# Kernel tuning notes

Measured on AMD Instinct MI355X. Metric: run time of the kernel, lower is better.

The kernel has to match this reference:

```python
import jax, jax.numpy as jnp
import numpy as np

N_ITEMS = 7000
N_USERS = 30000
N_NODES = N_ITEMS + N_USERS  # 37000
D = 128        # embed_dim == user_embed_dim
E = 400000     # num edges
R = 10         # n_relation (num ratings)
NB = 8         # num_bases
B = 512        # batch of conversations
L = 100        # max context items per sample


def setup_inputs() -> dict:
    key = jax.random.key(0)
    ks = jax.random.split(key, 16)
    # edges: item (source) -> user (target), disjoint id ranges as in load_data
    src = jax.random.randint(ks[0], (E,), 0, N_ITEMS)
    dst = jax.random.randint(ks[1], (E,), N_ITEMS, N_NODES)
    edge_index = jnp.stack([src, dst]).astype(jnp.int64)
    edge_type = jax.random.randint(ks[2], (E,), 0, R).astype(jnp.int64)

    def make_ctx(k1, k2):
        c = jax.random.randint(k1, (B, L), 0, N_ITEMS)
        drop = jax.random.uniform(k2, (B, L)) < 0.3  # -1 padding as in batch lists
        return jnp.where(drop, -1, c).astype(jnp.int64)

    ctx_init = make_ctx(ks[3], ks[4])
    ctx_resp = make_ctx(ks[5], ks[6])

    s = 0.02
    basis = jax.random.normal(ks[7], (NB, N_NODES, D), jnp.float32) * s
    comp = jax.random.normal(ks[8], (R, NB), jnp.float32) * s
    root = jax.random.normal(ks[9], (N_NODES, D), jnp.float32) * s
    bias = jnp.zeros((D,), jnp.float32)
    attn_a = jax.random.normal(ks[10], (D, D), jnp.float32) * s
    attn_b = jax.random.normal(ks[11], (D,), jnp.float32) * s
    fc1_w = jax.random.normal(ks[12], (D, D), jnp.float32) * s
    fc1_b = jnp.zeros((D,), jnp.float32)
    fc2_w = jax.random.normal(ks[13], (D, D), jnp.float32) * s
    fc2_b = jnp.zeros((D,), jnp.float32)
    efc1_w = jax.random.normal(ks[14], (2 * D, D), jnp.float32) * s
    efc1_b = jnp.zeros((D,), jnp.float32)
    efc2_w = jax.random.normal(ks[15], (D, D), jnp.float32) * s
    efc2_b = jnp.zeros((D,), jnp.float32)
    return dict(edge_index=edge_index, edge_type=edge_type, ctx_init=ctx_init,
                ctx_resp=ctx_resp, basis=basis, comp=comp, root=root, bias=bias,
                attn_a=attn_a, attn_b=attn_b, fc1_w=fc1_w, fc1_b=fc1_b,
                fc2_w=fc2_w, fc2_b=fc2_b, efc1_w=efc1_w, efc1_b=efc1_b,
                efc2_w=efc2_w, efc2_b=efc2_b)


def _rgcn(basis, comp, root, bias, edge_index, edge_type):
    # RGCNConv with x=None: per-edge message W_{r_e}[src_e], mean-aggregated
    # per (target, relation), summed over relations, plus root lookup + bias.
    src, dst = edge_index[0], edge_index[1]
    nb, n, d = basis.shape
    r = comp.shape[0]
    cpe = comp[edge_type]  # [E, NB]
    msg = jnp.zeros((src.shape[0], d), basis.dtype)
    for b in range(nb):  # small fixed basis count; avoids [E,NB,D] gather
        msg = msg + cpe[:, b:b + 1] * basis[b][src]
    seg = dst * r + edge_type  # per-(node, relation) segment for mean aggr
    sums = jax.ops.segment_sum(msg, seg, num_segments=n * r).reshape(n, r, d)
    cnt = jax.ops.segment_sum(jnp.ones_like(edge_type, basis.dtype), seg,
                              num_segments=n * r).reshape(n, r, 1)
    return root + bias + (sums / jnp.maximum(cnt, 1.0)).sum(axis=1)  # [N, D]


def _item_user_means(node_emb, edge_index):
    # mean over users connected to each item (edge_idx[1][edge_idx[0]==item])
    src, dst = edge_index[0], edge_index[1]
    isum = jax.ops.segment_sum(node_emb[dst], src, num_segments=N_ITEMS)
    icnt = jax.ops.segment_sum(jnp.ones_like(src, node_emb.dtype), src,
                               num_segments=N_ITEMS)
    item_mean = isum / jnp.maximum(icnt, 1.0)[:, None]  # [N_ITEMS, D]
    return item_mean, icnt > 0


def _attn_pool(ctx, item_mean, item_has_users, attn_a, attn_b):
    # SelfAttentionBatch over each sample's item reps (padding/-1 & degree-0
    # items masked out; all-empty samples -> zeros, as in original).
    valid = ctx >= 0
    idx = jnp.clip(ctx, 0, N_ITEMS - 1)
    h = item_mean[idx]                       # [B, L, D]
    valid = valid & item_has_users[idx]
    e = jnp.einsum('bld,d->bl', jnp.tanh(jnp.einsum('bld,de->ble', h, attn_a)),
                   attn_b)
    attn = jax.nn.softmax(jnp.where(valid, e, -1e9), axis=-1)
    attn = jnp.where(valid, attn, 0.0)
    return jnp.einsum('bl,bld->bd', attn, h)  # [B, D]


def _project(x, w1, b1, w2, b2):
    # fc1 -> relu -> fc2 -> relu (as in _project_user_interaction_*)
    return jax.nn.relu(jax.nn.relu(x @ w1 + b1) @ w2 + b2)


def reference(edge_index, edge_type, ctx_init, ctx_resp, basis, comp, root,
              bias, attn_a, attn_b, fc1_w, fc1_b, fc2_w, fc2_b, efc1_w,
              efc1_b, efc2_w, efc2_b):
    node_emb = _rgcn(basis, comp, root, bias, edge_index, edge_type)
    item_mean, item_has = _item_user_means(node_emb, edge_index)
    p_init = _project(_attn_pool(ctx_init, item_mean, item_has, attn_a, attn_b),
                      fc1_w, fc1_b, fc2_w, fc2_b)
    p_resp = _project(_attn_pool(ctx_resp, item_mean, item_has, attn_a, attn_b),
                      fc1_w, fc1_b, fc2_w, fc2_b)
    both = jnp.concatenate([p_init, p_resp], axis=1)  # [B, 2D]
    profile = _project(both, efc1_w, efc1_b, efc2_w, efc2_b)  # [B, D]
    return profile, p_init, p_resp
```

## Files before the change

### kernel.cpp

```cpp
#include <hip/hip_runtime.h>
#include <math.h>

typedef unsigned int uint;

#define N_ITEMS 7000
#define N_NODES 37000
#define N_USERS 30000
#define DIM     128
#define HD      64
#define NREL    10
#define NBASES  8
#define BATCH   512
#define CTXL    100
#define E_MAX   400000

#define OFF_CNT    0
#define OFF_ICNT   (OFF_CNT + N_USERS * NREL)
#define OFF_UCNT   (OFF_ICNT + N_ITEMS)
#define ZERO_ELEMS (OFF_UCNT + N_USERS)
#define OFF_ICUR   ZERO_ELEMS
#define OFF_UCUR   (OFF_ICUR + N_ITEMS)
#define OFF_ICSR   (OFF_UCUR + N_USERS)
#define OFF_UCSR   (OFF_ICSR + E_MAX)
#define OFF_WC     (OFF_UCSR + E_MAX)
#define OFF_ACC    (OFF_WC + NREL * N_ITEMS * HD)
#define OFF_MEAN   (OFF_ACC + N_USERS * HD)
#define OFF_SCORE  (OFF_MEAN + N_ITEMS * HD)

__device__ __forceinline__ float2 bf2f(uint p) {
  float2 r;
  r.x = __uint_as_float(p << 16);
  r.y = __uint_as_float(p & 0xffff0000u);
  return r;
}
__device__ __forceinline__ uint f2bf(float x, float y) {
  uint a = __float_as_uint(x), b = __float_as_uint(y);
  a += 0x7fffu + ((a >> 16) & 1u);
  b += 0x7fffu + ((b >> 16) & 1u);
  return (a >> 16) | (b & 0xffff0000u);
}

__device__ __forceinline__ float wave_sum(float v) {
#pragma unroll
  for (int o = 1; o < 64; o <<= 1) v += __shfl_xor(v, o, 64);
  return v;
}
__device__ __forceinline__ float wave_max(float v) {
#pragma unroll
  for (int o = 1; o < 64; o <<= 1) v = fmaxf(v, __shfl_xor(v, o, 64));
  return v;
}

__global__ __launch_bounds__(HD) void k_combine(const float* __restrict__ basis,
                                                const float* __restrict__ comp,
                                                uint* __restrict__ Wc) {
  int i = blockIdx.x, t = threadIdx.x;
  float2 bb[NBASES];
#pragma unroll
  for (int b = 0; b < NBASES; ++b)
    bb[b] = ((const float2*)(basis + ((size_t)b * N_NODES + i) * DIM))[t];
#pragma unroll
  for (int r = 0; r < NREL; ++r) {
    float sx = 0.f, sy = 0.f;
#pragma unroll
    for (int b = 0; b < NBASES; ++b) {
      float c = comp[r * NBASES + b];
      sx = fmaf(c, bb[b].x, sx);
      sy = fmaf(c, bb[b].y, sy);
    }
    Wc[((size_t)r * N_ITEMS + i) * HD + t] = f2bf(sx, sy);
  }
}

__global__ __launch_bounds__(256) void k_count(const int* __restrict__ ei,
                                               const int* __restrict__ et, int E,
                                               int* __restrict__ cnt,
                                               int* __restrict__ icnt,
                                               int* __restrict__ ucnt) {
  int e = blockIdx.x * 256 + threadIdx.x;
  if (e >= E) return;
  int s = ei[e];
  int u0 = ei[E + e] - N_ITEMS;
  int t = et[e];
  atomicAdd(&cnt[u0 * NREL + t], 1);
  atomicAdd(&icnt[s], 1);
  atomicAdd(&ucnt[u0], 1);
}

__global__ __launch_bounds__(1024) void k_scan(const int* __restrict__ icnt,
                                               const int* __restrict__ ucnt,
                                               int* __restrict__ icur,
                                               int* __restrict__ ucur) {
  __shared__ int ss[1024];
  const int* in;
  int n;
  int* cur;
  if (blockIdx.x == 0) { in = icnt; n = N_ITEMS; cur = icur; }
  else                 { in = ucnt; n = N_USERS; cur = ucur; }
  int t = threadIdx.x;
  int chunk = (n + 1023) / 1024;
  int lo = t * chunk, hi = lo + chunk;
  if (lo > n) lo = n;
  if (hi > n) hi = n;
  int s = 0;
  for (int i = lo; i < hi; ++i) s += in[i];
  ss[t] = s;
  __syncthreads();
  for (int o = 1; o < 1024; o <<= 1) {
    int v = (t >= o) ? ss[t - o] : 0;
    __syncthreads();
    ss[t] += v;
    __syncthreads();
  }
  int base = (t > 0) ? ss[t - 1] : 0;
  for (int i = lo; i < hi; ++i) { cur[i] = base; base += in[i]; }
}

__global__ __launch_bounds__(256) void k_fill(const int* __restrict__ ei,
                                              const int* __restrict__ et, int E,
                                              int* __restrict__ icur,
                                              int* __restrict__ ucur,
                                              int* __restrict__ icsr,
                                              int* __restrict__ ucsr) {
  int e = blockIdx.x * 256 + threadIdx.x;
  if (e >= E) return;
  int s = ei[e];
  int u0 = ei[E + e] - N_ITEMS;
  int t = et[e];
  icsr[atomicAdd(&icur[s], 1)] = u0;
  ucsr[atomicAdd(&ucur[u0], 1)] = s | (t << 16);
}

__global__ __launch_bounds__(HD) void k_useragg(const int* __restrict__ ucnt,
                                                const int* __restrict__ ucur,
                                                const int* __restrict__ ucsr,
                                                const int* __restrict__ cnt,
                                                const uint* __restrict__ Wc,
                                                const float* __restrict__ root,
                                                uint* __restrict__ acc) {
  __shared__ float wrow[NREL];
  __shared__ int sedge[HD];
  int u = blockIdx.x, t = threadIdx.x;
  if (t < NREL) {
    int c = cnt[u * NREL + t];
    wrow[t] = (c > 0) ? 1.0f / (float)c : 0.0f;
  }
  int deg = ucnt[u];
  int base = ucur[u] - deg;
  float2 a0 = {0.f, 0.f}, a1 = {0.f, 0.f}, a2 = {0.f, 0.f}, a3 = {0.f, 0.f};
  for (int j0 = 0; j0 < deg; j0 += HD) {
    int m = deg - j0;
    if (m > HD) m = HD;
    __syncthreads();
    if (t < m) sedge[t] = ucsr[base + j0 + t];
    __syncthreads();
    int j = 0;
    for (; j + 4 <= m; j += 4) {
      int p0 = sedge[j], p1 = sedge[j + 1], p2 = sedge[j + 2], p3 = sedge[j + 3];
      uint q0 = Wc[(size_t)((p0 >> 16) * N_ITEMS + (p0 & 0xffff)) * HD + t];
      uint q1 = Wc[(size_t)((p1 >> 16) * N_ITEMS + (p1 & 0xffff)) * HD + t];
      uint q2 = Wc[(size_t)((p2 >> 16) * N_ITEMS + (p2 & 0xffff)) * HD + t];
      uint q3 = Wc[(size_t)((p3 >> 16) * N_ITEMS + (p3 & 0xffff)) * HD + t];
      float w0 = wrow[p0 >> 16], w1 = wrow[p1 >> 16];
      float w2 = wrow[p2 >> 16], w3 = wrow[p3 >> 16];
      float2 f0 = bf2f(q0), f1 = bf2f(q1), f2 = bf2f(q2), f3 = bf2f(q3);
      a0.x = fmaf(w0, f0.x, a0.x); a0.y = fmaf(w0, f0.y, a0.y);
      a1.x = fmaf(w1, f1.x, a1.x); a1.y = fmaf(w1, f1.y, a1.y);
      a2.x = fmaf(w2, f2.x, a2.x); a2.y = fmaf(w2, f2.y, a2.y);
      a3.x = fmaf(w3, f3.x, a3.x); a3.y = fmaf(w3, f3.y, a3.y);
    }
    for (; j < m; ++j) {
      int p = sedge[j];
      uint q = Wc[(size_t)((p >> 16) * N_ITEMS + (p & 0xffff)) * HD + t];
      float w = wrow[p >> 16];
      float2 f = bf2f(q);
      a0.x = fmaf(w, f.x, a0.x); a0.y = fmaf(w, f.y, a0.y);
    }
  }
  float2 r = ((const float2*)(root + (size_t)(N_ITEMS + u) * DIM))[t];
  r.x += a0.x + a1.x + a2.x + a3.x;
  r.y += a0.y + a1.y + a2.y + a3.y;
  acc[(size_t)u * HD + t] = f2bf(r.x, r.y);
}

__global__ __launch_bounds__(HD) void k_itemagg(const int* __restrict__ icnt,
                                                const int* __restrict__ icur,
                                                const int* __restrict__ icsr,
                                                const uint* __restrict__ acc,
                                                const float* __restrict__ bias,
                                                const float* __restrict__ attn_a,
                                                const float* __restrict__ attn_b,
                                                uint* __restrict__ mean,
                                                float* __restrict__ score) {
  __shared__ int sedge[HD];
  __shared__ float sm[DIM];
  int i = blockIdx.x, t = threadIdx.x;
  int deg = icnt[i];
  int base = icur[i] - deg;
  float2 a0 = {0.f, 0.f}, a1 = {0.f, 0.f}, a2 = {0.f, 0.f}, a3 = {0.f, 0.f};
  for (int j0 = 0; j0 < deg; j0 += HD) {
    int m = deg - j0;
    if (m > HD) m = HD;
    __syncthreads();
    if (t < m) sedge[t] = icsr[base + j0 + t];
    __syncthreads();
    int j = 0;
    for (; j + 4 <= m; j += 4) {
      uint q0 = acc[(size_t)sedge[j] * HD + t];
      uint q1 = acc[(size_t)sedge[j + 1] * HD + t];
      uint q2 = acc[(size_t)sedge[j + 2] * HD + t];
      uint q3 = acc[(size_t)sedge[j + 3] * HD + t];
      float2 f0 = bf2f(q0), f1 = bf2f(q1), f2 = bf2f(q2), f3 = bf2f(q3);
      a0.x += f0.x; a0.y += f0.y;
      a1.x += f1.x; a1.y += f1.y;
      a2.x += f2.x; a2.y += f2.y;
      a3.x += f3.x; a3.y += f3.y;
    }
    for (; j < m; ++j) {
      float2 f = bf2f(acc[(size_t)sedge[j] * HD + t]);
      a0.x += f.x; a0.y += f.y;
    }
  }
  float2 mv = {0.f, 0.f};
  if (deg > 0) {
    float inv = 1.0f / (float)deg;
    float2 bvec = ((const float2*)bias)[t];
    mv.x = (a0.x + a1.x + a2.x + a3.x) * inv + bvec.x;
    mv.y = (a0.y + a1.y + a2.y + a3.y) * inv + bvec.y;
  }
  mean[(size_t)i * HD + t] = f2bf(mv.x, mv.y);
  sm[2 * t] = mv.x;
  sm[2 * t + 1] = mv.y;
  __syncthreads();
  float z0 = 0.f, z1 = 0.f;
#pragma unroll 8
  for (int k = 0; k < DIM; ++k) {
    float2 w = ((const float2*)(attn_a + (size_t)k * DIM))[t];
    float h = sm[k];
    z0 = fmaf(h, w.x, z0);
    z1 = fmaf(h, w.y, z1);
  }
  float2 ab = ((const float2*)attn_b)[t];
  float v = wave_sum(tanhf(z0) * ab.x + tanhf(z1) * ab.y);
  if (t == 0) score[i] = (deg > 0) ? v : -1e9f;
}

__global__ __launch_bounds__(HD) void k_pool(const int* __restrict__ ctx0,
                                             const int* __restrict__ ctx1,
                                             const uint* __restrict__ mean,
                                             const float* __restrict__ score,
                                             const float* __restrict__ fc1_w,
                                             const float* __restrict__ fc1_b,
                                             const float* __restrict__ fc2_w,
                                             const float* __restrict__ fc2_b,
                                             float* __restrict__ out) {
  __shared__ float shw[CTXL];
  __shared__ int shi[CTXL];
  __shared__ float shv[DIM];
  int b = blockIdx.x & (BATCH - 1);
  int c = blockIdx.x >> 9;
  int t = threadIdx.x;
  const int* cx = (c == 0 ? ctx0 : ctx1) + (size_t)b * CTXL;

  int id0 = cx[t];
  float e0 = (id0 >= 0) ? score[id0] : -1e9f;
  int id1 = -1;
  float e1 = -3.0e38f;
  if (t + HD < CTXL) {
    id1 = cx[t + HD];
    e1 = (id1 >= 0) ? score[id1] : -1e9f;
  }
  float m = wave_max(fmaxf(e0, e1));
  float x0 = expf(e0 - m);
  float x1 = (t + HD < CTXL) ? expf(e1 - m) : 0.f;
  float inv = 1.0f / wave_sum(x0 + x1);
  shw[t] = (id0 >= 0) ? x0 * inv : 0.f;
  shi[t] = (id0 >= 0) ? id0 : 0;
  if (t + HD < CTXL) {
    shw[t + HD] = (id1 >= 0) ? x1 * inv : 0.f;
    shi[t + HD] = (id1 >= 0) ? id1 : 0;
  }
  __syncthreads();

  float2 a0 = {0.f, 0.f}, a1 = {0.f, 0.f}, a2 = {0.f, 0.f}, a3 = {0.f, 0.f};
#pragma unroll 5
  for (int l = 0; l < CTXL; l += 4) {
    float w0 = shw[l], w1 = shw[l + 1], w2 = shw[l + 2], w3 = shw[l + 3];
    uint q0 = mean[(size_t)shi[l] * HD + t];
    uint q1 = mean[(size_t)shi[l + 1] * HD + t];
    uint q2 = mean[(size_t)shi[l + 2] * HD + t];
    uint q3 = mean[(size_t)shi[l + 3] * HD + t];
    float2 f0 = bf2f(q0), f1 = bf2f(q1), f2 = bf2f(q2), f3 = bf2f(q3);
    a0.x = fmaf(w0, f0.x, a0.x); a0.y = fmaf(w0, f0.y, a0.y);
    a1.x = fmaf(w1, f1.x, a1.x); a1.y = fmaf(w1, f1.y, a1.y);
    a2.x = fmaf(w2, f2.x, a2.x); a2.y = fmaf(w2, f2.y, a2.y);
    a3.x = fmaf(w3, f3.x, a3.x); a3.y = fmaf(w3, f3.y, a3.y);
  }
  __syncthreads();
  shv[2 * t] = a0.x + a1.x + a2.x + a3.x;
  shv[2 * t + 1] = a0.y + a1.y + a2.y + a3.y;
  __syncthreads();

  float2 z = ((const float2*)fc1_b)[t];
#pragma unroll 8
  for (int k = 0; k < DIM; ++k) {
    float2 w = ((const float2*)(fc1_w + (size_t)k * DIM))[t];
    float h = shv[k];
    z.x = fmaf(h, w.x, z.x);
    z.y = fmaf(h, w.y, z.y);
  }
  z.x = fmaxf(z.x, 0.f);
  z.y = fmaxf(z.y, 0.f);
  __syncthreads();
  shv[2 * t] = z.x;
  shv[2 * t + 1] = z.y;
  __syncthreads();

  float2 z2 = ((const float2*)fc2_b)[t];
#pragma unroll 8
  for (int k = 0; k < DIM; ++k) {
    float2 w = ((const float2*)(fc2_w + (size_t)k * DIM))[t];
    float h = shv[k];
    z2.x = fmaf(h, w.x, z2.x);
    z2.y = fmaf(h, w.y, z2.y);
  }
  z2.x = fmaxf(z2.x, 0.f);
  z2.y = fmaxf(z2.y, 0.f);
  ((float2*)(out + (size_t)(1 + c) * BATCH * DIM + (size_t)b * DIM))[t] = z2;
}

__global__ __launch_bounds__(HD) void k_profile(const float* __restrict__ efc1_w,
                                                const float* __restrict__ efc1_b,
                                                const float* __restrict__ efc2_w,
                                                const float* __restrict__ efc2_b,
                                                float* __restrict__ out) {
  __shared__ float shv[2 * DIM];
  __shared__ float sh2[DIM];
  int b = blockIdx.x, t = threadIdx.x;
  float2 p0 = ((const float2*)(out + (size_t)BATCH * DIM + (size_t)b * DIM))[t];
  float2 p1 = ((const float2*)(out + (size_t)2 * BATCH * DIM + (size_t)b * DIM))[t];
  shv[2 * t] = p0.x;
  shv[2 * t + 1] = p0.y;
  shv[DIM + 2 * t] = p1.x;
  shv[DIM + 2 * t + 1] = p1.y;
  __syncthreads();
  float2 z = ((const float2*)efc1_b)[t];
#pragma unroll 8
  for (int k = 0; k < 2 * DIM; ++k) {
    float2 w = ((const float2*)(efc1_w + (size_t)k * DIM))[t];
    float h = shv[k];
    z.x = fmaf(h, w.x, z.x);
    z.y = fmaf(h, w.y, z.y);
  }
  z.x = fmaxf(z.x, 0.f);
  z.y = fmaxf(z.y, 0.f);
  __syncthreads();
  sh2[2 * t] = z.x;
  sh2[2 * t + 1] = z.y;
  __syncthreads();
  float2 z2 = ((const float2*)efc2_b)[t];
#pragma unroll 8
  for (int k = 0; k < DIM; ++k) {
    float2 w = ((const float2*)(efc2_w + (size_t)k * DIM))[t];
    float h = sh2[k];
    z2.x = fmaf(h, w.x, z2.x);
    z2.y = fmaf(h, w.y, z2.y);
  }
  z2.x = fmaxf(z2.x, 0.f);
  z2.y = fmaxf(z2.y, 0.f);
  ((float2*)(out + (size_t)b * DIM))[t] = z2;
}

extern "C" void kernel_launch(void* const* d_in, const int* in_sizes, int n_in,
                              void* d_out, int out_size, void* d_ws, size_t ws_size,
                              hipStream_t stream) {
  const int*   ei     = (const int*)d_in[0];
  const int*   et     = (const int*)d_in[1];
  const int*   ctx0   = (const int*)d_in[2];
  const int*   ctx1   = (const int*)d_in[3];
  const float* basis  = (const float*)d_in[4];
  const float* comp   = (const float*)d_in[5];
  const float* root   = (const float*)d_in[6];
  const float* bias   = (const float*)d_in[7];
  const float* attn_a = (const float*)d_in[8];
  const float* attn_b = (const float*)d_in[9];
  const float* fc1_w  = (const float*)d_in[10];
  const float* fc1_b  = (const float*)d_in[11];
  const float* fc2_w  = (const float*)d_in[12];
  const float* fc2_b  = (const float*)d_in[13];
  const float* efc1_w = (const float*)d_in[14];
  const float* efc1_b = (const float*)d_in[15];
  const float* efc2_w = (const float*)d_in[16];
  const float* efc2_b = (const float*)d_in[17];
  float* out = (float*)d_out;

  const int E = in_sizes[1];

  float* ws   = (float*)d_ws;
  int*  cnt   = (int*)(ws + OFF_CNT);
  int*  icnt  = (int*)(ws + OFF_ICNT);
  int*  ucnt  = (int*)(ws + OFF_UCNT);
  int*  icur  = (int*)(ws + OFF_ICUR);
  int*  ucur  = (int*)(ws + OFF_UCUR);
  int*  icsr  = (int*)(ws + OFF_ICSR);
  int*  ucsr  = (int*)(ws + OFF_UCSR);
  uint* Wc    = (uint*)(ws + OFF_WC);
  uint* acc   = (uint*)(ws + OFF_ACC);
  uint* mean  = (uint*)(ws + OFF_MEAN);
  float* score = ws + OFF_SCORE;

  hipMemsetAsync(d_ws, 0, (size_t)ZERO_ELEMS * sizeof(float), stream);

  k_combine<<<N_ITEMS, HD, 0, stream>>>(basis, comp, Wc);
  k_count<<<(E + 255) / 256, 256, 0, stream>>>(ei, et, E, cnt, icnt, ucnt);
  k_scan<<<2, 1024, 0, stream>>>(icnt, ucnt, icur, ucur);
  k_fill<<<(E + 255) / 256, 256, 0, stream>>>(ei, et, E, icur, ucur, icsr, ucsr);
  k_useragg<<<N_USERS, HD, 0, stream>>>(ucnt, ucur, ucsr, cnt, Wc, root, acc);
  k_itemagg<<<N_ITEMS, HD, 0, stream>>>(icnt, icur, icsr, acc, bias, attn_a, attn_b,
                                        mean, score);
  k_pool<<<2 * BATCH, HD, 0, stream>>>(ctx0, ctx1, mean, score, fc1_w, fc1_b,
                                       fc2_w, fc2_b, out);
  k_profile<<<BATCH, HD, 0, stream>>>(efc1_w, efc1_b, efc2_w, efc2_b, out);
}
```

Before: 481.3 us.

## Fuse all pipeline stages into one cooperative persistent kernel with grid syncs

Replaces the eight separate launches with a single cooperative kernel of 512 blocks that loops over work per wavefront and separates stages with grid.sync(). The two-block scan becomes a multi-block tiled scan, and the gathers plus small matvecs switch from shared memory to wave shuffles with deeper unrolling of independent accumulators. The aim is to remove launch gaps and per-block sync overhead. In exchange, each stage runs on a fixed grid, which may leave gather-heavy stages with less parallelism or latency hiding than before. The old multi-kernel path is kept as a fallback when cooperative occupancy is insufficient.

```diff
diff --git a/kernel.cpp b/kernel.cpp
--- a/kernel.cpp
+++ b/kernel.cpp
@@ -1,6 +1,8 @@
 #include <hip/hip_runtime.h>
+#include <hip/hip_cooperative_groups.h>
 #include <math.h>
 
+namespace cg = cooperative_groups;
 typedef unsigned int uint;
 
 #define N_ITEMS 7000
@@ -14,13 +16,24 @@
 #define CTXL    100
 #define E_MAX   400000
 
+#define NBLK    512
+#define NTHR    256
+#define NTHREADS_TOT (NBLK * NTHR)
+#define NW      (NTHREADS_TOT / 64)
+
+#define NT_I 28
+#define NT_U 118
+#define NT   (NT_I + NT_U)
+
 #define OFF_CNT    0
 #define OFF_ICNT   (OFF_CNT + N_USERS * NREL)
 #define OFF_UCNT   (OFF_ICNT + N_ITEMS)
 #define ZERO_ELEMS (OFF_UCNT + N_USERS)
 #define OFF_ICUR   ZERO_ELEMS
 #define OFF_UCUR   (OFF_ICUR + N_ITEMS)
-#define OFF_ICSR   (OFF_UCUR + N_USERS)
+#define OFF_TSUM   (OFF_UCUR + N_USERS)
+#define OFF_TOFF   (OFF_TSUM + 256)
+#define OFF_ICSR   (OFF_TOFF + 256)
 #define OFF_UCSR   (OFF_ICSR + E_MAX)
 #define OFF_WC     (OFF_UCSR + E_MAX)
 #define OFF_ACC    (OFF_WC + NREL * N_ITEMS * HD)
@@ -49,6 +62,388 @@
 #pragma unroll
   for (int o = 1; o < 64; o <<= 1) v = fmaxf(v, __shfl_xor(v, o, 64));
   return v;
+}
+__device__ __forceinline__ int wave_sum_i(int v) {
+#pragma unroll
+  for (int o = 1; o < 64; o <<= 1) v += __shfl_xor(v, o, 64);
+  return v;
+}
+
+struct Args {
+  const int* ei;
+  const int* et;
+  const int* ctx0;
+  const int* ctx1;
+  const float* basis;
+  const float* comp;
+  const float* root;
+  const float* bias;
+  const float* attn_a;
+  const float* attn_b;
+  const float* fc1_w;
+  const float* fc1_b;
+  const float* fc2_w;
+  const float* fc2_b;
+  const float* efc1_w;
+  const float* efc1_b;
+  const float* efc2_w;
+  const float* efc2_b;
+  float* out;
+  float* ws;
+  int E;
+};
+
+__global__ __launch_bounds__(NTHR, 2) void k_fused(Args a) {
+  cg::grid_group grid = cg::this_grid();
+  __shared__ int ss[256];
+  __shared__ int s4[4];
+
+  const int tid  = threadIdx.x;
+  const int gtid = blockIdx.x * NTHR + tid;
+  const int wid  = gtid >> 6;
+  const int lane = gtid & 63;
+  const int E = a.E;
+
+  int*  cnt   = (int*)(a.ws + OFF_CNT);
+  int*  icnt  = (int*)(a.ws + OFF_ICNT);
+  int*  ucnt  = (int*)(a.ws + OFF_UCNT);
+  int*  icur  = (int*)(a.ws + OFF_ICUR);
+  int*  ucur  = (int*)(a.ws + OFF_UCUR);
+  int*  tsum  = (int*)(a.ws + OFF_TSUM);
+  int*  toff  = (int*)(a.ws + OFF_TOFF);
+  int*  icsr  = (int*)(a.ws + OFF_ICSR);
+  int*  ucsr  = (int*)(a.ws + OFF_UCSR);
+  uint* Wc    = (uint*)(a.ws + OFF_WC);
+  uint* acc   = (uint*)(a.ws + OFF_ACC);
+  uint* mean  = (uint*)(a.ws + OFF_MEAN);
+  float* score = a.ws + OFF_SCORE;
+
+  const float2* basis2 = (const float2*)a.basis;
+  const float2* root2  = (const float2*)a.root;
+  const float2* bias2  = (const float2*)a.bias;
+  const float2* attnA2 = (const float2*)a.attn_a;
+  const float2* attnB2 = (const float2*)a.attn_b;
+  const float2* fc1w2  = (const float2*)a.fc1_w;
+  const float2* fc1b2  = (const float2*)a.fc1_b;
+  const float2* fc2w2  = (const float2*)a.fc2_w;
+  const float2* fc2b2  = (const float2*)a.fc2_b;
+  const float2* e1w2   = (const float2*)a.efc1_w;
+  const float2* e1b2   = (const float2*)a.efc1_b;
+  const float2* e2w2   = (const float2*)a.efc2_w;
+  const float2* e2b2   = (const float2*)a.efc2_b;
+  float2* out2 = (float2*)a.out;
+
+  for (int i = wid; i < N_ITEMS; i += NW) {
+    float2 bb[NBASES];
+#pragma unroll
+    for (int b = 0; b < NBASES; ++b)
+      bb[b] = basis2[((size_t)b * N_NODES + i) * HD + lane];
+#pragma unroll
+    for (int r = 0; r < NREL; ++r) {
+      float sx = 0.f, sy = 0.f;
+#pragma unroll
+      for (int b = 0; b < NBASES; ++b) {
+        float c = a.comp[r * NBASES + b];
+        sx = fmaf(c, bb[b].x, sx);
+        sy = fmaf(c, bb[b].y, sy);
+      }
+      Wc[((size_t)r * N_ITEMS + i) * HD + lane] = f2bf(sx, sy);
+    }
+  }
+  for (int e = gtid; e < E; e += NTHREADS_TOT) {
+    int s  = a.ei[e];
+    int u0 = a.ei[E + e] - N_ITEMS;
+    int t  = a.et[e];
+    atomicAdd(&cnt[u0 * NREL + t], 1);
+    atomicAdd(&icnt[s], 1);
+    atomicAdd(&ucnt[u0], 1);
+  }
+  grid.sync();
+
+  if (blockIdx.x < NT) {
+    int b = blockIdx.x;
+    bool isU = (b >= NT_I);
+    const int* arr = isU ? ucnt : icnt;
+    int n = isU ? N_USERS : N_ITEMS;
+    int idx = (isU ? (b - NT_I) : b) * 256 + tid;
+    int v = (idx < n) ? arr[idx] : 0;
+    int wsum = wave_sum_i(v);
+    if ((tid & 63) == 0) s4[tid >> 6] = wsum;
+    __syncthreads();
+    if (tid == 0) tsum[b] = s4[0] + s4[1] + s4[2] + s4[3];
+  }
+  grid.sync();
+
+  if (blockIdx.x == 0) {
+    int li = -1;
+    if (tid < NT_I) li = tid;
+    else if (tid < NT) li = 128 + (tid - NT_I);
+    ss[tid] = 0;
+    __syncthreads();
+    if (li >= 0) ss[li] = tsum[tid];
+    __syncthreads();
+    for (int o = 1; o < 128; o <<= 1) {
+      int x = 0;
+      if (tid >= o && ((tid < 128) == ((tid - o) < 128))) x = ss[tid - o];
+      __syncthreads();
+      ss[tid] += x;
+      __syncthreads();
+    }
+    if (li >= 0) {
+      int excl = 0;
+      if (li != 0 && li != 128) excl = ss[li - 1];
+      toff[tid] = excl;
+    }
+  }
+  grid.sync();
+
+  if (blockIdx.x < NT) {
+    int b = blockIdx.x;
+    bool isU = (b >= NT_I);
+    const int* arr = isU ? ucnt : icnt;
+    int* cur = isU ? ucur : icur;
+    int n = isU ? N_USERS : N_ITEMS;
+    int idx = (isU ? (b - NT_I) : b) * 256 + tid;
+    int v = (idx < n) ? arr[idx] : 0;
+    ss[tid] = v;
+    __syncthreads();
+    for (int o = 1; o < 256; o <<= 1) {
+      int x = (tid >= o) ? ss[tid - o] : 0;
+      __syncthreads();
+      ss[tid] += x;
+      __syncthreads();
+    }
+    if (idx < n) cur[idx] = ss[tid] - v + toff[b];
+  }
+  grid.sync();
+
+  for (int e = gtid; e < E; e += NTHREADS_TOT) {
+    int s  = a.ei[e];
+    int u0 = a.ei[E + e] - N_ITEMS;
+    int t  = a.et[e];
+    icsr[atomicAdd(&icur[s], 1)] = u0;
+    ucsr[atomicAdd(&ucur[u0], 1)] = s | (t << 16);
+  }
+  grid.sync();
+
+  for (int u = wid; u < N_USERS; u += NW) {
+    int deg  = ucnt[u];
+    int base = ucur[u] - deg;
+    float wl = 0.f;
+    if (lane < NREL) {
+      int c = cnt[u * NREL + lane];
+      wl = (c > 0) ? 1.0f / (float)c : 0.0f;
+    }
+    float2 av[8];
+#pragma unroll
+    for (int k = 0; k < 8; ++k) { av[k].x = 0.f; av[k].y = 0.f; }
+    for (int j0 = 0; j0 < deg; j0 += 64) {
+      int m = deg - j0;
+      if (m > 64) m = 64;
+      int pl = (lane < m) ? ucsr[base + j0 + lane] : 0;
+      int j = 0;
+      for (; j + 8 <= m; j += 8) {
+#pragma unroll
+        for (int k = 0; k < 8; ++k) {
+          int p = __shfl(pl, j + k);
+          int r = p >> 16;
+          float w = __shfl(wl, r);
+          uint q = Wc[(size_t)(r * N_ITEMS + (p & 0xffff)) * HD + lane];
+          float2 f = bf2f(q);
+          av[k].x = fmaf(w, f.x, av[k].x);
+          av[k].y = fmaf(w, f.y, av[k].y);
+        }
+      }
+      for (; j < m; ++j) {
+        int p = __shfl(pl, j);
+        int r = p >> 16;
+        float w = __shfl(wl, r);
+        uint q = Wc[(size_t)(r * N_ITEMS + (p & 0xffff)) * HD + lane];
+        float2 f = bf2f(q);
+        av[0].x = fmaf(w, f.x, av[0].x);
+        av[0].y = fmaf(w, f.y, av[0].y);
+      }
+    }
+    float2 rt = root2[(size_t)(N_ITEMS + u) * HD + lane];
+    rt.x += ((av[0].x + av[1].x) + (av[2].x + av[3].x)) +
+            ((av[4].x + av[5].x) + (av[6].x + av[7].x));
+    rt.y += ((av[0].y + av[1].y) + (av[2].y + av[3].y)) +
+            ((av[4].y + av[5].y) + (av[6].y + av[7].y));
+    acc[(size_t)u * HD + lane] = f2bf(rt.x, rt.y);
+  }
+  grid.sync();
+
+  for (int i = wid; i < N_ITEMS; i += NW) {
+    int deg  = icnt[i];
+    int base = icur[i] - deg;
+    float2 av[8];
+#pragma unroll
+    for (int k = 0; k < 8; ++k) { av[k].x = 0.f; av[k].y = 0.f; }
+    for (int j0 = 0; j0 < deg; j0 += 64) {
+      int m = deg - j0;
+      if (m > 64) m = 64;
+      int pl = (lane < m) ? icsr[base + j0 + lane] : 0;
+      int j = 0;
+      for (; j + 8 <= m; j += 8) {
+#pragma unroll
+        for (int k = 0; k < 8; ++k) {
+          int u0 = __shfl(pl, j + k);
+          float2 f = bf2f(acc[(size_t)u0 * HD + lane]);
+          av[k].x += f.x;
+          av[k].y += f.y;
+        }
+      }
+      for (; j < m; ++j) {
+        int u0 = __shfl(pl, j);
+        float2 f = bf2f(acc[(size_t)u0 * HD + lane]);
+        av[0].x += f.x;
+        av[0].y += f.y;
+      }
+    }
+    float sx = ((av[0].x + av[1].x) + (av[2].x + av[3].x)) +
+               ((av[4].x + av[5].x) + (av[6].x + av[7].x));
+    float sy = ((av[0].y + av[1].y) + (av[2].y + av[3].y)) +
+               ((av[4].y + av[5].y) + (av[6].y + av[7].y));
+    float2 mv = {0.f, 0.f};
+    if (deg > 0) {
+      float inv = 1.0f / (float)deg;
+      float2 bv = bias2[lane];
+      mv.x = sx * inv + bv.x;
+      mv.y = sy * inv + bv.y;
+    }
+    mean[(size_t)i * HD + lane] = f2bf(mv.x, mv.y);
+    float z0 = 0.f, z1 = 0.f;
+#pragma unroll 8
+    for (int k2 = 0; k2 < HD; ++k2) {
+      float hx = __shfl(mv.x, k2);
+      float hy = __shfl(mv.y, k2);
+      float2 w0 = attnA2[(size_t)(2 * k2) * HD + lane];
+      float2 w1 = attnA2[(size_t)(2 * k2 + 1) * HD + lane];
+      z0 = fmaf(hx, w0.x, z0); z1 = fmaf(hx, w0.y, z1);
+      z0 = fmaf(hy, w1.x, z0); z1 = fmaf(hy, w1.y, z1);
+    }
+    float2 ab = attnB2[lane];
+    float v = wave_sum(tanhf(z0) * ab.x + tanhf(z1) * ab.y);
+    if (lane == 0) score[i] = (deg > 0) ? v : -1e9f;
+  }
+  grid.sync();
+
+  for (int sd = wid; sd < 2 * BATCH; sd += NW) {
+    int b = sd & (BATCH - 1);
+    int c = sd >> 9;
+    const int* cx = (c ? a.ctx1 : a.ctx0) + (size_t)b * CTXL;
+    int id0 = cx[lane];
+    float e0 = (id0 >= 0) ? score[id0] : -1e9f;
+    int id1 = -1;
+    float e1 = -3.0e38f;
+    if (lane < CTXL - 64) {
+      id1 = cx[64 + lane];
+      e1 = (id1 >= 0) ? score[id1] : -1e9f;
+    }
+    float mx = wave_max(fmaxf(e0, e1));
+    float x0 = expf(e0 - mx);
+    float x1 = (lane < CTXL - 64) ? expf(e1 - mx) : 0.f;
+    float inv = 1.0f / wave_sum(x0 + x1);
+    float w0 = (id0 >= 0) ? x0 * inv : 0.f;
+    float w1 = (id1 >= 0) ? x1 * inv : 0.f;
+    int i0 = (id0 >= 0) ? id0 : 0;
+    int i1 = (id1 >= 0) ? id1 : 0;
+
+    float2 av[4];
+#pragma unroll
+    for (int k = 0; k < 4; ++k) { av[k].x = 0.f; av[k].y = 0.f; }
+    for (int j = 0; j < 64; j += 4) {
+#pragma unroll
+      for (int k = 0; k < 4; ++k) {
+        int ii = __shfl(i0, j + k);
+        float ww = __shfl(w0, j + k);
+        float2 f = bf2f(mean[(size_t)ii * HD + lane]);
+        av[k].x = fmaf(ww, f.x, av[k].x);
+        av[k].y = fmaf(ww, f.y, av[k].y);
+      }
+    }
+    for (int j = 0; j < CTXL - 64; j += 4) {
+#pragma unroll
+      for (int k = 0; k < 4; ++k) {
+        int ii = __shfl(i1, j + k);
+        float ww = __shfl(w1, j + k);
+        float2 f = bf2f(mean[(size_t)ii * HD + lane]);
+        av[k].x = fmaf(ww, f.x, av[k].x);
+        av[k].y = fmaf(ww, f.y, av[k].y);
+      }
+    }
+    float2 pool;
+    pool.x = (av[0].x + av[1].x) + (av[2].x + av[3].x);
+    pool.y = (av[0].y + av[1].y) + (av[2].y + av[3].y);
+
+    float2 z = fc1b2[lane];
+#pragma unroll 8
+    for (int k2 = 0; k2 < HD; ++k2) {
+      float hx = __shfl(pool.x, k2);
+      float hy = __shfl(pool.y, k2);
+      float2 wa = fc1w2[(size_t)(2 * k2) * HD + lane];
+      float2 wb = fc1w2[(size_t)(2 * k2 + 1) * HD + lane];
+      z.x = fmaf(hx, wa.x, z.x); z.y = fmaf(hx, wa.y, z.y);
+      z.x = fmaf(hy, wb.x, z.x); z.y = fmaf(hy, wb.y, z.y);
+    }
+    z.x = fmaxf(z.x, 0.f);
+    z.y = fmaxf(z.y, 0.f);
+
+    float2 z2 = fc2b2[lane];
+#pragma unroll 8
+    for (int k2 = 0; k2 < HD; ++k2) {
+      float hx = __shfl(z.x, k2);
+      float hy = __shfl(z.y, k2);
+      float2 wa = fc2w2[(size_t)(2 * k2) * HD + lane];
+      float2 wb = fc2w2[(size_t)(2 * k2 + 1) * HD + lane];
+      z2.x = fmaf(hx, wa.x, z2.x); z2.y = fmaf(hx, wa.y, z2.y);
+      z2.x = fmaf(hy, wb.x, z2.x); z2.y = fmaf(hy, wb.y, z2.y);
+    }
+    z2.x = fmaxf(z2.x, 0.f);
+    z2.y = fmaxf(z2.y, 0.f);
+    out2[((size_t)(1 + c) * BATCH + b) * HD + lane] = z2;
+  }
+  grid.sync();
+
+  for (int b = wid; b < BATCH; b += NW) {
+    float2 p0 = out2[((size_t)BATCH + b) * HD + lane];
+    float2 p1 = out2[((size_t)2 * BATCH + b) * HD + lane];
+    float2 z = e1b2[lane];
+#pragma unroll 8
+    for (int k2 = 0; k2 < HD; ++k2) {
+      float hx = __shfl(p0.x, k2);
+      float hy = __shfl(p0.y, k2);
+      float2 wa = e1w2[(size_t)(2 * k2) * HD + lane];
+      float2 wb = e1w2[(size_t)(2 * k2 + 1) * HD + lane];
+      z.x = fmaf(hx, wa.x, z.x); z.y = fmaf(hx, wa.y, z.y);
+      z.x = fmaf(hy, wb.x, z.x); z.y = fmaf(hy, wb.y, z.y);
+    }
+#pragma unroll 8
+    for (int k2 = 0; k2 < HD; ++k2) {
+      float hx = __shfl(p1.x, k2);
+      float hy = __shfl(p1.y, k2);
+      float2 wa = e1w2[(size_t)(DIM + 2 * k2) * HD + lane];
+      float2 wb = e1w2[(size_t)(DIM + 2 * k2 + 1) * HD + lane];
+      z.x = fmaf(hx, wa.x, z.x); z.y = fmaf(hx, wa.y, z.y);
+      z.x = fmaf(hy, wb.x, z.x); z.y = fmaf(hy, wb.y, z.y);
+    }
+    z.x = fmaxf(z.x, 0.f);
+    z.y = fmaxf(z.y, 0.f);
+
+    float2 z2 = e2b2[lane];
+#pragma unroll 8
+    for (int k2 = 0; k2 < HD; ++k2) {
+      float hx = __shfl(z.x, k2);
+      float hy = __shfl(z.y, k2);
+      float2 wa = e2w2[(size_t)(2 * k2) * HD + lane];
+      float2 wb = e2w2[(size_t)(2 * k2 + 1) * HD + lane];
+      z2.x = fmaf(hx, wa.x, z2.x); z2.y = fmaf(hx, wa.y, z2.y);
+      z2.x = fmaf(hy, wb.x, z2.x); z2.y = fmaf(hy, wb.y, z2.y);
+    }
+    z2.x = fmaxf(z2.x, 0.f);
+    z2.y = fmaxf(z2.y, 0.f);
+    out2[(size_t)b * HD + lane] = z2;
+  }
 }
 
 __global__ __launch_bounds__(HD) void k_combine(const float* __restrict__ basis,
@@ -138,49 +533,50 @@
                                                 const uint* __restrict__ Wc,
                                                 const float* __restrict__ root,
                                                 uint* __restrict__ acc) {
-  __shared__ float wrow[NREL];
-  __shared__ int sedge[HD];
-  int u = blockIdx.x, t = threadIdx.x;
-  if (t < NREL) {
-    int c = cnt[u * NREL + t];
-    wrow[t] = (c > 0) ? 1.0f / (float)c : 0.0f;
-  }
+  int u = blockIdx.x, lane = threadIdx.x;
   int deg = ucnt[u];
   int base = ucur[u] - deg;
-  float2 a0 = {0.f, 0.f}, a1 = {0.f, 0.f}, a2 = {0.f, 0.f}, a3 = {0.f, 0.f};
-  for (int j0 = 0; j0 < deg; j0 += HD) {
+  float wl = 0.f;
+  if (lane < NREL) {
+    int c = cnt[u * NREL + lane];
+    wl = (c > 0) ? 1.0f / (float)c : 0.0f;
+  }
+  float2 av[8];
+#pragma unroll
+  for (int k = 0; k < 8; ++k) { av[k].x = 0.f; av[k].y = 0.f; }
+  for (int j0 = 0; j0 < deg; j0 += 64) {
     int m = deg - j0;
-    if (m > HD) m = HD;
-    __syncthreads();
-    if (t < m) sedge[t] = ucsr[base + j0 + t];
-    __syncthreads();
+    if (m > 64) m = 64;
+    int pl = (lane < m) ? ucsr[base + j0 + lane] : 0;
     int j = 0;
-    for (; j + 4 <= m; j += 4) {
-      int p0 = sedge[j], p1 = sedge[j + 1], p2 = sedge[j + 2], p3 = sedge[j + 3];
-      uint q0 = Wc[(size_t)((p0 >> 16) * N_ITEMS + (p0 & 0xffff)) * HD + t];
-      uint q1 = Wc[(size_t)((p1 >> 16) * N_ITEMS + (p1 & 0xffff)) * HD + t];
-      uint q2 = Wc[(size_t)((p2 >> 16) * N_ITEMS + (p2 & 0xffff)) * HD + t];
-      uint q3 = Wc[(size_t)((p3 >> 16) * N_ITEMS + (p3 & 0xffff)) * HD + t];
-      float w0 = wrow[p0 >> 16], w1 = wrow[p1 >> 16];
-      float w2 = wrow[p2 >> 16], w3 = wrow[p3 >> 16];
-      float2 f0 = bf2f(q0), f1 = bf2f(q1), f2 = bf2f(q2), f3 = bf2f(q3);
-      a0.x = fmaf(w0, f0.x, a0.x); a0.y = fmaf(w0, f0.y, a0.y);
-      a1.x = fmaf(w1, f1.x, a1.x); a1.y = fmaf(w1, f1.y, a1.y);
-      a2.x = fmaf(w2, f2.x, a2.x); a2.y = fmaf(w2, f2.y, a2.y);
-      a3.x = fmaf(w3, f3.x, a3.x); a3.y = fmaf(w3, f3.y, a3.y);
+    for (; j + 8 <= m; j += 8) {
+#pragma unroll
+      for (int k = 0; k < 8; ++k) {
+        int p = __shfl(pl, j + k);
+        int r = p >> 16;
+        float w = __shfl(wl, r);
+        uint q = Wc[(size_t)(r * N_ITEMS + (p & 0xffff)) * HD + lane];
+        float2 f = bf2f(q);
+        av[k].x = fmaf(w, f.x, av[k].x);
+        av[k].y = fmaf(w, f.y, av[k].y);
+      }
     }
     for (; j < m; ++j) {
-      int p = sedge[j];
-      uint q = Wc[(size_t)((p >> 16) * N_ITEMS + (p & 0xffff)) * HD + t];
-      float w = wrow[p >> 16];
+      int p = __shfl(pl, j);
+      int r = p >> 16;
+      float w = __shfl(wl, r);
+      uint q = Wc[(size_t)(r * N_ITEMS + (p & 0xffff)) * HD + lane];
       float2 f = bf2f(q);
-      a0.x = fmaf(w, f.x, a0.x); a0.y = fmaf(w, f.y, a0.y);
-    }
-  }
-  float2 r = ((const float2*)(root + (size_t)(N_ITEMS + u) * DIM))[t];
-  r.x += a0.x + a1.x + a2.x + a3.x;
-  r.y += a0.y + a1.y + a2.y + a3.y;
-  acc[(size_t)u * HD + t] = f2bf(r.x, r.y);
+      av[0].x = fmaf(w, f.x, av[0].x);
+      av[0].y = fmaf(w, f.y, av[0].y);
+    }
+  }
+  float2 rt = ((const float2*)(root + (size_t)(N_ITEMS + u) * DIM))[lane];
+  rt.x += ((av[0].x + av[1].x) + (av[2].x + av[3].x)) +
+          ((av[4].x + av[5].x) + (av[6].x + av[7].x));
+  rt.y += ((av[0].y + av[1].y) + (av[2].y + av[3].y)) +
+          ((av[4].y + av[5].y) + (av[6].y + av[7].y));
+  acc[(size_t)u * HD + lane] = f2bf(rt.x, rt.y);
 }
 
 __global__ __launch_bounds__(HD) void k_itemagg(const int* __restrict__ icnt,
@@ -192,57 +588,58 @@
                                                 const float* __restrict__ attn_b,
                                                 uint* __restrict__ mean,
                                                 float* __restrict__ score) {
-  __shared__ int sedge[HD];
-  __shared__ float sm[DIM];
-  int i = blockIdx.x, t = threadIdx.x;
+  int i = blockIdx.x, lane = threadIdx.x;
   int deg = icnt[i];
   int base = icur[i] - deg;
-  float2 a0 = {0.f, 0.f}, a1 = {0.f, 0.f}, a2 = {0.f, 0.f}, a3 = {0.f, 0.f};
-  for (int j0 = 0; j0 < deg; j0 += HD) {
+  float2 av[8];
+#pragma unroll
+  for (int k = 0; k < 8; ++k) { av[k].x = 0.f; av[k].y = 0.f; }
+  for (int j0 = 0; j0 < deg; j0 += 64) {
     int m = deg - j0;
-    if (m > HD) m = HD;
-    __syncthreads();
-    if (t < m) sedge[t] = icsr[base + j0 + t];
-    __syncthreads();
+    if (m > 64) m = 64;
+    int pl = (lane < m) ? icsr[base + j0 + lane] : 0;
     int j = 0;
-    for (; j + 4 <= m; j += 4) {
-      uint q0 = acc[(size_t)sedge[j] * HD + t];
-      uint q1 = acc[(size_t)sedge[j + 1] * HD + t];
-      uint q2 = acc[(size_t)sedge[j + 2] * HD + t];
-      uint q3 = acc[(size_t)sedge[j + 3] * HD + t];
-      float2 f0 = bf2f(q0), f1 = bf2f(q1), f2 = bf2f(q2), f3 = bf2f(q3);
-      a0.x += f0.x; a0.y += f0.y;
-      a1.x += f1.x; a1.y += f1.y;
-      a2.x += f2.x; a2.y += f2.y;
-      a3.x += f3.x; a3.y += f3.y;
+    for (; j + 8 <= m; j += 8) {
+#pragma unroll
+      for (int k = 0; k < 8; ++k) {
+        int u0 = __shfl(pl, j + k);
+        float2 f = bf2f(acc[(size_t)u0 * HD + lane]);
+        av[k].x += f.x;
+        av[k].y += f.y;
+      }
     }
     for (; j < m; ++j) {
-      float2 f = bf2f(acc[(size_t)sedge[j] * HD + t]);
-      a0.x += f.x; a0.y += f.y;
-    }
-  }
+      int u0 = __shfl(pl, j);
+      float2 f = bf2f(acc[(size_t)u0 * HD + lane]);
+      av[0].x += f.x;
+      av[0].y += f.y;
+    }
+  }
+  float sx = ((av[0].x + av[1].x) + (av[2].x + av[3].x)) +
+             ((av[4].x + av[5].x) + (av[6].x + av[7].x));
+  float sy = ((av[0].y + av[1].y) + (av[2].y + av[3].y)) +
+             ((av[4].y + av[5].y) + (av[6].y + av[7].y));
   float2 mv = {0.f, 0.f};
   if (deg > 0) {
     float inv = 1.0f / (float)deg;
-    float2 bvec = ((const float2*)bias)[t];
-    mv.x = (a0.x + a1.x + a2.x + a3.x) * inv + bvec.x;
-    mv.y = (a0.y + a1.y + a2.y + a3.y) * inv + bvec.y;
-  }
-  mean[(size_t)i * HD + t] = f2bf(mv.x, mv.y);
-  sm[2 * t] = mv.x;
-  sm[2 * t + 1] = mv.y;
-  __syncthreads();
+    float2 bv = ((const float2*)bias)[lane];
+    mv.x = sx * inv + bv.x;
+    mv.y = sy * inv + bv.y;
+  }
+  mean[(size_t)i * HD + lane] = f2bf(mv.x, mv.y);
   float z0 = 0.f, z1 = 0.f;
 #pragma unroll 8
-  for (int k = 0; k < DIM; ++k) {
-    float2 w = ((const float2*)(attn_a + (size_t)k * DIM))[t];
-    float h = sm[k];
-    z0 = fmaf(h, w.x, z0);
-    z1 = fmaf(h, w.y, z1);
-  }
-  float2 ab = ((const float2*)attn_b)[t];
+  for (int k2 = 0; k2 < HD; ++k2) {
+    float hx = __shfl(mv.x, k2);
+    float hy = __shfl(mv.y, k2);
+    float2 w0 = ((const float2*)attn_a)[(size_t)(2 * k2) * HD + lane];
+    float2 w1 = ((const float2*)attn_a)[(size_t)(2 * k2 + 1) * HD + lane];
+    z0 = fmaf(hx, w0.x, z0); z1 = fmaf(hx, w0.y, z1);
+    z0 = fmaf(hy, w1.x, z0); z1 = fmaf(hy, w1.y, z1);
+  }
+  float2 ab = ((const float2*)attn_b)[lane];
   float v = wave_sum(tanhf(z0) * ab.x + tanhf(z1) * ab.y);
-  if (t == 0) score[i] = (deg > 0) ? v : -1e9f;
+  if (lane == 0) score[i] = (deg > 0) ? v : -1e9f;
 }
 
 __global__ __launch_bounds__(HD) void k_pool(const int* __restrict__ ctx0,
@@ -254,79 +651,80 @@
                                              const float* __restrict__ fc2_w,
                                              const float* __restrict__ fc2_b,
                                              float* __restrict__ out) {
-  __shared__ float shw[CTXL];
-  __shared__ int shi[CTXL];
-  __shared__ float shv[DIM];
   int b = blockIdx.x & (BATCH - 1);
   int c = blockIdx.x >> 9;
-  int t = threadIdx.x;
-  const int* cx = (c == 0 ? ctx0 : ctx1) + (size_t)b * CTXL;
-
-  int id0 = cx[t];
+  int lane = threadIdx.x;
+  const int* cx = (c ? ctx1 : ctx0) + (size_t)b * CTXL;
+  int id0 = cx[lane];
   float e0 = (id0 >= 0) ? score[id0] : -1e9f;
   int id1 = -1;
   float e1 = -3.0e38f;
-  if (t + HD < CTXL) {
-    id1 = cx[t + HD];
+  if (lane < CTXL - 64) {
+    id1 = cx[64 + lane];
     e1 = (id1 >= 0) ? score[id1] : -1e9f;
   }
-  float m = wave_max(fmaxf(e0, e1));
-  float x0 = expf(e0 - m);
-  float x1 = (t + HD < CTXL) ? expf(e1 - m) : 0.f;
+  float mx = wave_max(fmaxf(e0, e1));
+  float x0 = expf(e0 - mx);
+  float x1 = (lane < CTXL - 64) ? expf(e1 - mx) : 0.f;
   float inv = 1.0f / wave_sum(x0 + x1);
-  shw[t] = (id0 >= 0) ? x0 * inv : 0.f;
-  shi[t] = (id0 >= 0) ? id0 : 0;
-  if (t + HD < CTXL) {
-    shw[t + HD] = (id1 >= 0) ? x1 * inv : 0.f;
-    shi[t + HD] = (id1 >= 0) ? id1 : 0;
-  }
-  __syncthreads();
-
-  float2 a0 = {0.f, 0.f}, a1 = {0.f, 0.f}, a2 = {0.f, 0.f}, a3 = {0.f, 0.f};
-#pragma unroll 5
-  for (int l = 0; l < CTXL; l += 4) {
-    float w0 = shw[l], w1 = shw[l + 1], w2 = shw[l + 2], w3 = shw[l + 3];
-    uint q0 = mean[(size_t)shi[l] * HD + t];
-    uint q1 = mean[(size_t)shi[l + 1] * HD + t];
-    uint q2 = mean[(size_t)shi[l + 2] * HD + t];
-    uint q3 = mean[(size_t)shi[l + 3] * HD + t];
-    float2 f0 = bf2f(q0), f1 = bf2f(q1), f2 = bf2f(q2), f3 = bf2f(q3);
-    a0.x = fmaf(w0, f0.x, a0.x); a0.y = fmaf(w0, f0.y, a0.y);
-    a1.x = fmaf(w1, f1.x, a1.x); a1.y = fmaf(w1, f1.y, a1.y);
-    a2.x = fmaf(w2, f2.x, a2.x); a2.y = fmaf(w2, f2.y, a2.y);
-    a3.x = fmaf(w3, f3.x, a3.x); a3.y = fmaf(w3, f3.y, a3.y);
-  }
-  __syncthreads();
-  shv[2 * t] = a0.x + a1.x + a2.x + a3.x;
-  shv[2 * t + 1] = a0.y + a1.y + a2.y + a3.y;
-  __syncthreads();
-
-  float2 z = ((const float2*)fc1_b)[t];
-#pragma unroll 8
-  for (int k = 0; k < DIM; ++k) {
-    float2 w = ((const float2*)(fc1_w + (size_t)k * DIM))[t];
-    float h = shv[k];
-    z.x = fmaf(h, w.x, z.x);
-    z.y = fmaf(h, w.y, z.y);
+  float w0 = (id0 >= 0) ? x0 * inv : 0.f;
+  float w1 = (id1 >= 0) ? x1 * inv : 0.f;
+  int i0 = (id0 >= 0) ? id0 : 0;
+  int i1 = (id1 >= 0) ? id1 : 0;
+
+  float2 av[4];
+#pragma unroll
+  for (int k = 0; k < 4; ++k) { av[k].x = 0.f; av[k].y = 0.f; }
+  for (int j = 0; j < 64; j += 4) {
+#pragma unroll
+    for (int k = 0; k < 4; ++k) {
+      int ii = __shfl(i0, j + k);
+      float ww = __shfl(w0, j + k);
+      float2 f = bf2f(mean[(size_t)ii * HD + lane]);
+      av[k].x = fmaf(ww, f.x, av[k].x);
+      av[k].y = fmaf(ww, f.y, av[k].y);
+    }
+  }
+  for (int j = 0; j < CTXL - 64; j += 4) {
+#pragma unroll
+    for (int k = 0; k < 4; ++k) {
+      int ii = __shfl(i1, j + k);
+      float ww = __shfl(w1, j + k);
+      float2 f = bf2f(mean[(size_t)ii * HD + lane]);
+      av[k].x = fmaf(ww, f.x, av[k].x);
+      av[k].y = fmaf(ww, f.y, av[k].y);
+    }
+  }
+  float2 pool;
+  pool.x = (av[0].x + av[1].x) + (av[2].x + av[3].x);
+  pool.y = (av[0].y + av[1].y) + (av[2].y + av[3].y);
+
+  float2 z = ((const float2*)fc1_b)[lane];
+#pragma unroll 8
+  for (int k2 = 0; k2 < HD; ++k2) {
+    float hx = __shfl(pool.x, k2);
+    float hy = __shfl(pool.y, k2);
+    float2 wa = ((const float2*)fc1_w)[(size_t)(2 * k2) * HD + lane];
+    float2 wb = ((const float2*)fc1_w)[(size_t)(2 * k2 + 1) * HD + lane];
+    z.x = fmaf(hx, wa.x, z.x); z.y = fmaf(hx, wa.y, z.y);
+    z.x = fmaf(hy, wb.x, z.x); z.y = fmaf(hy, wb.y, z.y);
   }
   z.x = fmaxf(z.x, 0.f);
   z.y = fmaxf(z.y, 0.f);
-  __syncthreads();
-  shv[2 * t] = z.x;
-  shv[2 * t + 1] = z.y;
-  __syncthreads();
-
-  float2 z2 = ((const float2*)fc2_b)[t];
-#pragma unroll 8
-  for (int k = 0; k < DIM; ++k) {
-    float2 w = ((const float2*)(fc2_w + (size_t)k * DIM))[t];
-    float h = shv[k];
-    z2.x = fmaf(h, w.x, z2.x);
-    z2.y = fmaf(h, w.y, z2.y);
+
+  float2 z2 = ((const float2*)fc2_b)[lane];
+#pragma unroll 8
+  for (int k2 = 0; k2 < HD; ++k2) {
+    float hx = __shfl(z.x, k2);
+    float hy = __shfl(z.y, k2);
+    float2 wa = ((const float2*)fc2_w)[(size_t)(2 * k2) * HD + lane];
+    float2 wb = ((const float2*)fc2_w)[(size_t)(2 * k2 + 1) * HD + lane];
+    z2.x = fmaf(hx, wa.x, z2.x); z2.y = fmaf(hx, wa.y, z2.y);
+    z2.x = fmaf(hy, wb.x, z2.x); z2.y = fmaf(hy, wb.y, z2.y);
   }
   z2.x = fmaxf(z2.x, 0.f);
   z2.y = fmaxf(z2.y, 0.f);
-  ((float2*)(out + (size_t)(1 + c) * BATCH * DIM + (size_t)b * DIM))[t] = z2;
+  ((float2*)out)[((size_t)(1 + c) * BATCH + b) * HD + lane] = z2;
 }
 
 __global__ __launch_bounds__(HD) void k_profile(const float* __restrict__ efc1_w,
@@ -334,91 +732,111 @@
                                                 const float* __restrict__ efc2_w,
                                                 const float* __restrict__ efc2_b,
                                                 float* __restrict__ out) {
-  __shared__ float shv[2 * DIM];
-  __shared__ float sh2[DIM];
-  int b = blockIdx.x, t = threadIdx.x;
-  float2 p0 = ((const float2*)(out + (size_t)BATCH * DIM + (size_t)b * DIM))[t];
-  float2 p1 = ((const float2*)(out + (size_t)2 * BATCH * DIM + (size_t)b * DIM))[t];
-  shv[2 * t] = p0.x;
-  shv[2 * t + 1] = p0.y;
-  shv[DIM + 2 * t] = p1.x;
-  shv[DIM + 2 * t + 1] = p1.y;
-  __syncthreads();
-  float2 z = ((const float2*)efc1_b)[t];
-#pragma unroll 8
-  for (int k = 0; k < 2 * DIM; ++k) {
-    float2 w = ((const float2*)(efc1_w + (size_t)k * DIM))[t];
-    float h = shv[k];
-    z.x = fmaf(h, w.x, z.x);
-    z.y = fmaf(h, w.y, z.y);
+  int b = blockIdx.x, lane = threadIdx.x;
+  float2* out2 = (float2*)out;
+  float2 p0 = out2[((size_t)BATCH + b) * HD + lane];
+  float2 p1 = out2[((size_t)2 * BATCH + b) * HD + lane];
+  float2 z = ((const float2*)efc1_b)[lane];
+#pragma unroll 8
+  for (int k2 = 0; k2 < HD; ++k2) {
+    float hx = __shfl(p0.x, k2);
+    float hy = __shfl(p0.y, k2);
+    float2 wa = ((const float2*)efc1_w)[(size_t)(2 * k2) * HD + lane];
+    float2 wb = ((const float2*)efc1_w)[(size_t)(2 * k2 + 1) * HD + lane];
+    z.x = fmaf(hx, wa.x, z.x); z.y = fmaf(hx, wa.y, z.y);
+    z.x = fmaf(hy, wb.x, z.x); z.y = fmaf(hy, wb.y, z.y);
+  }
+#pragma unroll 8
+  for (int k2 = 0; k2 < HD; ++k2) {
+    float hx = __shfl(p1.x, k2);
+    float hy = __shfl(p1.y, k2);
+    float2 wa = ((const float2*)efc1_w)[(size_t)(DIM + 2 * k2) * HD + lane];
+    float2 wb = ((const float2*)efc1_w)[(size_t)(DIM + 2 * k2 + 1) * HD + lane];
+    z.x = fmaf(hx, wa.x, z.x); z.y = fmaf(hx, wa.y, z.y);
+    z.x = fmaf(hy, wb.x, z.x); z.y = fmaf(hy, wb.y, z.y);
   }
   z.x = fmaxf(z.x, 0.f);
   z.y = fmaxf(z.y, 0.f);
-  __syncthreads();
-  sh2[2 * t] = z.x;
-  sh2[2 * t + 1] = z.y;
-  __syncthreads();
-  float2 z2 = ((const float2*)efc2_b)[t];
-#pragma unroll 8
-  for (int k = 0; k < DIM; ++k) {
-    float2 w = ((const float2*)(efc2_w + (size_t)k * DIM))[t];
-    float h = sh2[k];
-    z2.x = fmaf(h, w.x, z2.x);
-    z2.y = fmaf(h, w.y, z2.y);
+
+  float2 z2 = ((const float2*)efc2_b)[lane];
+#pragma unroll 8
+  for (int k2 = 0; k2 < HD; ++k2) {
+    float hx = __shfl(z.x, k2);
+    float hy = __shfl(z.y, k2);
+    float2 wa = ((const float2*)efc2_w)[(size_t)(2 * k2) * HD + lane];
+    float2 wb = ((const float2*)efc2_w)[(size_t)(2 * k2 + 1) * HD + lane];
+    z2.x = fmaf(hx, wa.x, z2.x); z2.y = fmaf(hx, wa.y, z2.y);
+    z2.x = fmaf(hy, wb.x, z2.x); z2.y = fmaf(hy, wb.y, z2.y);
   }
   z2.x = fmaxf(z2.x, 0.f);
   z2.y = fmaxf(z2.y, 0.f);
-  ((float2*)(out + (size_t)b * DIM))[t] = z2;
+  out2[(size_t)b * HD + lane] = z2;
 }
 
 extern "C" void kernel_launch(void* const* d_in, const int* in_sizes, int n_in,
                               void* d_out, int out_size, void* d_ws, size_t ws_size,
                               hipStream_t stream) {
-  const int*   ei     = (const int*)d_in[0];
-  const int*   et     = (const int*)d_in[1];
-  const int*   ctx0   = (const int*)d_in[2];
-  const int*   ctx1   = (const int*)d_in[3];
-  const float* basis  = (const float*)d_in[4];
-  const float* comp   = (const float*)d_in[5];
-  const float* root   = (const float*)d_in[6];
-  const float* bias   = (const float*)d_in[7];
-  const float* attn_a = (const float*)d_in[8];
-  const float* attn_b = (const float*)d_in[9];
-  const float* fc1_w  = (const float*)d_in[10];
-  const float* fc1_b  = (const float*)d_in[11];
-  const float* fc2_w  = (const float*)d_in[12];
-  const float* fc2_b  = (const float*)d_in[13];
-  const float* efc1_w = (const float*)d_in[14];
-  const float* efc1_b = (const float*)d_in[15];
-  const float* efc2_w = (const float*)d_in[16];
-  const float* efc2_b = (const float*)d_in[17];
-  float* out = (float*)d_out;
-
-  const int E = in_sizes[1];
-
-  float* ws   = (float*)d_ws;
-  int*  cnt   = (int*)(ws + OFF_CNT);
-  int*  icnt  = (int*)(ws + OFF_ICNT);
-  int*  ucnt  = (int*)(ws + OFF_UCNT);
-  int*  icur  = (int*)(ws + OFF_ICUR);
-  int*  ucur  = (int*)(ws + OFF_UCUR);
-  int*  icsr  = (int*)(ws + OFF_ICSR);
-  int*  ucsr  = (int*)(ws + OFF_UCSR);
-  uint* Wc    = (uint*)(ws + OFF_WC);
-  uint* acc   = (uint*)(ws + OFF_ACC);
-  uint* mean  = (uint*)(ws + OFF_MEAN);
-  float* score = ws + OFF_SCORE;
+  Args args;
+  args.ei     = (const int*)d_in[0];
+  args.et     = (const int*)d_in[1];
+  args.ctx0   = (const int*)d_in[2];
+  args.ctx1   = (const int*)d_in[3];
+  args.basis  = (const float*)d_in[4];
+  args.comp   = (const float*)d_in[5];
+  args.root   = (const float*)d_in[6];
+  args.bias   = (const float*)d_in[7];
+  args.attn_a = (const float*)d_in[8];
+  args.attn_b = (const float*)d_in[9];
+  args.fc1_w  = (const float*)d_in[10];
+  args.fc1_b  = (const float*)d_in[11];
+  args.fc2_w  = (const float*)d_in[12];
+  args.fc2_b  = (const float*)d_in[13];
+  args.efc1_w = (const float*)d_in[14];
+  args.efc1_b = (const float*)d_in[15];
+  args.efc2_w = (const float*)d_in[16];
+  args.efc2_b = (const float*)d_in[17];
+  args.out    = (float*)d_out;
+  args.ws     = (float*)d_ws;
+  args.E      = in_sizes[1];
 
   hipMemsetAsync(d_ws, 0, (size_t)ZERO_ELEMS * sizeof(float), stream);
 
-  k_combine<<<N_ITEMS, HD, 0, stream>>>(basis, comp, Wc);
-  k_count<<<(E + 255) / 256, 256, 0, stream>>>(ei, et, E, cnt, icnt, ucnt);
-  k_scan<<<2, 1024, 0, stream>>>(icnt, ucnt, icur, ucur);
-  k_fill<<<(E + 255) / 256, 256, 0, stream>>>(ei, et, E, icur, ucur, icsr, ucsr);
-  k_useragg<<<N_USERS, HD, 0, stream>>>(ucnt, ucur, ucsr, cnt, Wc, root, acc);
-  k_itemagg<<<N_ITEMS, HD, 0, stream>>>(icnt, icur, icsr, acc, bias, attn_a, attn_b,
-                                        mean, score);
-  k_pool<<<2 * BATCH, HD, 0, stream>>>(ctx0, ctx1, mean, score, fc1_w, fc1_b,
-                                       fc2_w, fc2_b, out);
-  k_profile<<<BATCH, HD, 0, stream>>>(efc1_w, efc1_b, efc2_w, efc2_b, out);
-}
+  int blocksPerCU = 0;
+  hipError_t qerr = hipOccupancyMaxActiveBlocksPerMultiprocessor(
+      &blocksPerCU, (const void*)k_fused, NTHR, 0);
+  bool useCoop = (qerr == hipSuccess) && (blocksPerCU * 256 >= NBLK);
+
+  if (useCoop) {
+    void* params[1] = {&args};
+    hipLaunchCooperativeKernel((const void*)k_fused, dim3(NBLK), dim3(NTHR),
+                               params, 0, stream);
+  } else {
+    const int E = args.E;
+    float* ws   = (float*)d_ws;
+    int*  cnt   = (int*)(ws + OFF_CNT);
+    int*  icnt  = (int*)(ws + OFF_ICNT);
+    int*  ucnt  = (int*)(ws + OFF_UCNT);
+    int*  icur  = (int*)(ws + OFF_ICUR);
+    int*  ucur  = (int*)(ws + OFF_UCUR);
+    int*  icsr  = (int*)(ws + OFF_ICSR);
+    int*  ucsr  = (int*)(ws + OFF_UCSR);
+    uint* Wc    = (uint*)(ws + OFF_WC);
+    uint* acc   = (uint*)(ws + OFF_ACC);
+    uint* mean  = (uint*)(ws + OFF_MEAN);
+    float* score = ws + OFF_SCORE;
+    float* out  = (float*)d_out;
+
+    k_combine<<<N_ITEMS, HD, 0, stream>>>(args.basis, args.comp, Wc);
+    k_count<<<(E + 255) / 256, 256, 0, stream>>>(args.ei, args.et, E, cnt, icnt, ucnt);
+    k_scan<<<2, 1024, 0, stream>>>(icnt, ucnt, icur, ucur);
+    k_fill<<<(E + 255) / 256, 256, 0, stream>>>(args.ei, args.et, E, icur, ucur, icsr, ucsr);
+    k_useragg<<<N_USERS, HD, 0, stream>>>(ucnt, ucur, ucsr, cnt, Wc, args.root, acc);
+    k_itemagg<<<N_ITEMS, HD, 0, stream>>>(icnt, icur, icsr, acc, args.bias,
+                                          args.attn_a, args.attn_b, mean, score);
+    k_pool<<<2 * BATCH, HD, 0, stream>>>(args.ctx0, args.ctx1, mean, score,
+                                         args.fc1_w, args.fc1_b, args.fc2_w,
+                                         args.fc2_b, out);
+    k_profile<<<BATCH, HD, 0, stream>>>(args.efc1_w, args.efc1_b, args.efc2_w,
+                                        args.efc2_b, out);
+  }
+}
```

Result: slower. 962.4 us (+100.0%).
